# Performance work log

Hardware: AMD Instinct MI355X
Metric: run time of the kernel (lower is better)

Reference implementation:

```python
import jax, jax.numpy as jnp
import numpy as np

B = 524288   # particles
H = 128      # hidden_size
E = 64       # embed_dim
NT = 512     # num trajectories
IN = 16 + 9 + E  # fc1 input dim = 89
EPS = 1e-6


def setup_inputs() -> dict:
    key = jax.random.key(0)
    ks = jax.random.split(key, 12)
    w = lambda k, shp, fan_in: (jax.random.normal(k, shp, dtype=jnp.float32)
                                / np.sqrt(fan_in).astype(np.float32))
    return {
        "F": jax.random.normal(ks[0], (B, 3, 3), dtype=jnp.float32),
        "C": jax.random.normal(ks[1], (B, 3, 3), dtype=jnp.float32),
        "traj_id": 7,
        "latent": jax.random.normal(ks[2], (NT, E), dtype=jnp.float32),
        "W1": w(ks[3], (IN, H), IN), "b1": jnp.zeros((H,), jnp.float32),
        "W2": w(ks[4], (H, H), H),   "b2": jnp.zeros((H,), jnp.float32),
        "W3": w(ks[5], (H, H), H),   "b3": jnp.zeros((H,), jnp.float32),
        "W4": w(ks[6], (H, H), H),   "b4": jnp.zeros((H,), jnp.float32),
        "W5": w(ks[7], (H, H), H),   "b5": jnp.zeros((H,), jnp.float32),
        "W6": w(ks[8], (H, H), H),   "b6": jnp.zeros((H,), jnp.float32),
        "W7": w(ks[9], (H, 9), H),   "b7": jnp.zeros((9,), jnp.float32),
    }


def _strain_features(F):
    # FFt: [B,3,3]; J = clamp(det F); J1 = clamp(F00); sigma: 3 singular values
    FFt = jnp.einsum('bij,bkj->bik', F, F)
    J = jnp.maximum(jnp.linalg.det(F), EPS)
    J1 = jnp.maximum(F[:, 0, 0], EPS)
    sigma = jnp.linalg.svd(F, compute_uv=False)  # descending, like torch.svd
    return jnp.concatenate([
        FFt.reshape(-1, 9),
        jnp.log(J)[:, None], sigma, J[:, None],
        jnp.log(J1)[:, None], J1[:, None],
    ], axis=-1)  # [B,16]


def reference(F, C, traj_id, latent,
              W1, b1, W2, b2, W3, b3, W4, b4, W5, b5, W6, b6, W7, b7):
    strain = _strain_features(F)                                   # [B,16]
    lat = jnp.broadcast_to(latent[traj_id], (F.shape[0], latent.shape[1]))
    x = jnp.concatenate([strain, C.reshape(-1, 9), lat], axis=-1)  # [B,89]
    g = lambda z: jax.nn.gelu(z, approximate=False)  # exact, matches torch GELU
    x = g(x @ W1 + b1)
    x = g(x @ W2 + b2)
    x = g(x @ W3 + b3)
    x = g(x @ W4 + b4)
    x = g(x @ W5 + b5)
    x = g(x @ W6 + b6)
    out = (x @ W7 + b7).reshape(-1, 3, 3)
    return 0.5 * (out + jnp.swapaxes(out, 1, 2))  # symmetric stress [B,3,3]
```

## Files before the change

### kernel.cpp

```cpp
#include <hip/hip_runtime.h>
#include <hip/hip_bf16.h>
#include <math.h>

#define BPART   524288
#define NBLK    (BPART / 128)
#define W7_OFF  98304
#define WB_N    102400
#define BIAS_N  800
#define PREP_N  (WB_N + BIAS_N)

typedef __bf16 bf16x8 __attribute__((ext_vector_type(8)));
typedef float  f32x16 __attribute__((ext_vector_type(16)));
typedef float  f32x4  __attribute__((ext_vector_type(4)));
typedef float  f32x2  __attribute__((ext_vector_type(2)));

#define MFMA __builtin_amdgcn_mfma_f32_32x32x16_bf16
#define UNROLL _Pragma("unroll")

union XU { unsigned u[4]; bf16x8 v; };

__device__ __forceinline__ unsigned short f2bf(float f) {
  union { float f; unsigned u; } v; v.f = f;
  unsigned r = v.u + 0x7fffu + ((v.u >> 16) & 1u);
  return (unsigned short)(r >> 16);
}
__device__ __forceinline__ unsigned pack_bf16(float a, float b) {
  unsigned ua = __builtin_bit_cast(unsigned, a) + 0x8000u;
  unsigned ub = __builtin_bit_cast(unsigned, b) + 0x8000u;
  return __builtin_amdgcn_perm(ub, ua, 0x07060302u);
}

__device__ __forceinline__ int sigma(int n) {
  int c = ((n >> 5) << 2) | ((n >> 3) & 3);
  return ((c >> 1) << 4) | (((n >> 2) & 1) << 3) | ((c & 1) << 2) | (n & 3);
}

__device__ __forceinline__ f32x2 pk_mul(f32x2 a, f32x2 b) {
  f32x2 d; asm("v_pk_mul_f32 %0, %1, %2" : "=v"(d) : "v"(a), "v"(b)); return d;
}
__device__ __forceinline__ f32x2 pk_fma(f32x2 a, f32x2 b, f32x2 c) {
  f32x2 d; asm("v_pk_fma_f32 %0, %1, %2, %3" : "=v"(d) : "v"(a), "v"(b), "v"(c)); return d;
}
__device__ __forceinline__ f32x2 gelu2(f32x2 z) {
  const f32x2 c1 = {0.1029432f, 0.1029432f};
  const f32x2 c0 = {2.30220818f, 2.30220818f};
  f32x2 z2 = pk_mul(z, z);
  f32x2 t  = pk_fma(z2, c1, c0);
  f32x2 yp = pk_mul(z, t);
  float e0 = __builtin_amdgcn_exp2f(-yp.x);
  float e1 = __builtin_amdgcn_exp2f(-yp.y);
  float r0 = __builtin_amdgcn_rcpf(e0 + 1.0f);
  float r1 = __builtin_amdgcn_rcpf(e1 + 1.0f);
  f32x2 g; g.x = z.x * r0; g.y = z.y * r1;
  return g;
}
__device__ __forceinline__ void cp16(const void* g, void* l) {
  __builtin_amdgcn_global_load_lds(
      (const __attribute__((address_space(1))) void*)g,
      (__attribute__((address_space(3))) void*)l, 16, 0, 0);
}

__global__ void prep_weights(
    const float* __restrict__ W1, const float* __restrict__ W2,
    const float* __restrict__ W3, const float* __restrict__ W4,
    const float* __restrict__ W5, const float* __restrict__ W6,
    const float* __restrict__ W7,
    const float* __restrict__ b1, const float* __restrict__ b2,
    const float* __restrict__ b3, const float* __restrict__ b4,
    const float* __restrict__ b5, const float* __restrict__ b6,
    const float* __restrict__ b7,
    unsigned short* __restrict__ wsb, float* __restrict__ wsf)
{
  int idx = blockIdx.x * 256 + threadIdx.x;
  if (idx < WB_N) {
    unsigned short v = 0;
    if (idx < W7_OFF) {
      int l = idx >> 14;
      int o = idx & 16383;
      int n = o >> 7, e = o & 127;
      int k = (((e >> 3) ^ (n & 7)) << 3) | (e & 7);
      int sn = sigma(n);
      const float* W = (l==0)?W1:(l==1)?W2:(l==2)?W3:(l==3)?W4:(l==4)?W5:W6;
      float x = (l == 0) ? ((k < 89) ? W[k*128 + sn] : 0.0f)
                         : W[k*128 + sn];
      v = f2bf(x);
    } else {
      int o = idx - W7_OFF;
      int n = o >> 7, e = o & 127;
      int k = (((e >> 3) ^ (n & 7)) << 3) | (e & 7);
      int sn = sigma(n);
      v = (sn < 9) ? f2bf(W7[k*9 + sn]) : (unsigned short)0;
    }
    wsb[idx] = v;
  } else if (idx < PREP_N) {
    int r = idx - WB_N;
    float x;
    if (r < 768) {
      int l = r >> 7, n = r & 127;
      const float* bb = (l==0)?b1:(l==1)?b2:(l==2)?b3:(l==3)?b4:(l==4)?b5:b6;
      x = bb[sigma(n)];
    } else {
      int n = r - 768;
      int sn = sigma(n);
      x = (sn < 9) ? b7[sn] : 0.0f;
    }
    wsf[r] = x;
  }
}

#define MFMA_LAYER(NKK)                                                       \
  {                                                                           \
    const float* bls_ = (const float*)((const char*)wt_s + 32768);            \
    UNROLL                                                                    \
    for (int kk = 0; kk < (NKK); ++kk) {                                      \
      XU x_;                                                                  \
      x_.u[0] = xw[4*kk+0]; x_.u[1] = xw[4*kk+1];                             \
      x_.u[2] = xw[4*kk+2]; x_.u[3] = xw[4*kk+3];                             \
      const int ch_ = ((2*kk + lk) ^ x7) << 3;                                \
      UNROLL                                                                  \
      for (int tn = 0; tn < 4; ++tn) {                                        \
        bf16x8 w_ = *(const bf16x8*)&wt_s[tn*4096 + rb0 + ch_];               \
        if (kk == 0) {                                                        \
          f32x16 cf_;                                                         \
          UNROLL                                                              \
          for (int qq = 0; qq < 4; ++qq) {                                    \
            f32x4 b4_ = *(const f32x4*)&bls_[tn*32 + qq*8 + lk*4];            \
            cf_[4*qq+0] = b4_[0]; cf_[4*qq+1] = b4_[1];                       \
            cf_[4*qq+2] = b4_[2]; cf_[4*qq+3] = b4_[3];                       \
          }                                                                   \
          acc[tn] = MFMA(w_, x_.v, cf_, 0, 0, 0);                             \
        } else {                                                              \
          acc[tn] = MFMA(w_, x_.v, acc[tn], 0, 0, 0);                         \
        }                                                                     \
      }                                                                       \
    }                                                                         \
  }

#define GELU_EPILOGUE                                                         \
  UNROLL                                                                      \
  for (int c = 0; c < 16; ++c) {                                              \
    const int tn_ = c >> 2, q_ = c & 3, t_ = c >> 1, h_ = c & 1;              \
    f32x2 za_, zb_;                                                           \
    za_.x = acc[tn_][4*q_+0]; za_.y = acc[tn_][4*q_+1];                       \
    zb_.x = acc[tn_][4*q_+2]; zb_.y = acc[tn_][4*q_+3];                       \
    f32x2 ga_ = gelu2(za_);                                                   \
    f32x2 gb_ = gelu2(zb_);                                                   \
    xw[4*t_ + 2*h_ + 0] = pack_bf16(ga_.x, ga_.y);                            \
    xw[4*t_ + 2*h_ + 1] = pack_bf16(gb_.x, gb_.y);                            \
  }

__global__ __launch_bounds__(256, 4) void stress_mlp(
    const float* __restrict__ F, const float* __restrict__ Cmat,
    const int* __restrict__ traj, const float* __restrict__ latent,
    const unsigned short* __restrict__ wst, const float* __restrict__ wsf,
    float* __restrict__ out)
{
  __shared__ __align__(16) unsigned short wt_s[128 * 128 + 256];

  const int tid  = threadIdx.x;
  const int lane = tid & 63;
  const int wid  = tid >> 6;
  const int lm   = lane & 31;
  const int lk   = lane >> 5;
  const int x7   = lm & 7;
  const int rb0  = lm << 7;
  const int pbase = (int)blockIdx.x << 7;
  const int p    = pbase + (wid << 5) + lm;

  {
    const char* src = (const char*)wst;
    char* dst = (char*)wt_s;
    UNROLL
    for (int i = 0; i < 8; ++i)
      cp16(src + i*4096 + tid*16, dst + i*4096 + tid*16);
    if (tid < 32) cp16((const char*)wsf + tid*16, dst + 32768 + tid*16);
  }

  unsigned xw[32];

  {
    const float* Fp = F + (size_t)p * 9;
    float f[9];
    UNROLL
    for (int i = 0; i < 9; ++i) f[i] = Fp[i];
    float fft[9];
    UNROLL
    for (int i = 0; i < 3; ++i)
      UNROLL
      for (int k = 0; k < 3; ++k)
        fft[i*3+k] = f[i*3]*f[k*3] + f[i*3+1]*f[k*3+1] + f[i*3+2]*f[k*3+2];
    const float* lat = latent + (size_t)traj[0] * 64;

    if (lk == 0) {
      xw[0] = pack_bf16(fft[0], fft[1]);
      xw[1] = pack_bf16(fft[2], fft[3]);
      xw[2] = pack_bf16(fft[4], fft[5]);
      xw[3] = pack_bf16(fft[6], fft[7]);
      const float* Cp = Cmat + (size_t)p * 9;
      UNROLL
      for (int i = 0; i < 4; ++i) xw[4+i] = pack_bf16(Cp[2*i], Cp[2*i+1]);
      UNROLL
      for (int t = 0; t < 4; ++t) {
        const float* lb = lat + 7 + 16*t;
        UNROLL
        for (int i = 0; i < 4; ++i) xw[8 + 4*t + i] = pack_bf16(lb[2*i], lb[2*i+1]);
      }
    } else {
      float det = f[0]*(f[4]*f[8]-f[5]*f[7]) - f[1]*(f[3]*f[8]-f[5]*f[6])
                + f[2]*(f[3]*f[7]-f[4]*f[6]);
      float J  = fmaxf(det, 1e-6f);
      float J1 = fmaxf(f[0], 1e-6f);
      float a00=fft[0], a01=fft[1], a02=fft[2], a11=fft[4], a12=fft[5], a22=fft[8];
      float q  = (a00+a11+a22) * (1.0f/3.0f);
      float d0 = a00-q, d1 = a11-q, d2 = a22-q;
      float p2 = d0*d0 + d1*d1 + d2*d2 + 2.0f*(a01*a01 + a02*a02 + a12*a12);
      float e0, e1, e2;
      if (p2 < 1e-14f) { e0 = e1 = e2 = q; }
      else {
        float pp  = sqrtf(p2 * (1.0f/6.0f));
        float inv = 1.0f / pp;
        float b00=d0*inv, b11=d1*inv, b22=d2*inv, b01=a01*inv, b02=a02*inv, b12=a12*inv;
        float detb = b00*(b11*b22-b12*b12) - b01*(b01*b22-b12*b02) + b02*(b01*b12-b11*b02);
        float rr = 0.5f * detb;
        rr = fminf(fmaxf(rr, -1.0f), 1.0f);
        float pr = acosf(rr) * (1.0f / (3.0f * 6.2831853071795864f));
        e0 = q + 2.0f*pp*__builtin_amdgcn_cosf(pr);
        e2 = q + 2.0f*pp*__builtin_amdgcn_cosf(pr + (1.0f/3.0f));
        e1 = 3.0f*q - e0 - e2;
      }
      float s0 = sqrtf(fmaxf(e0, 0.f));
      float s1 = sqrtf(fmaxf(e1, 0.f));
      float s2 = sqrtf(fmaxf(e2, 0.f));
      xw[0] = pack_bf16(fft[8], logf(J));
      xw[1] = pack_bf16(s0, s1);
      xw[2] = pack_bf16(s2, J);
      xw[3] = pack_bf16(logf(J1), J1);
      float c8 = Cmat[(size_t)p*9 + 8];
      xw[4] = pack_bf16(c8, lat[0]);
      xw[5] = pack_bf16(lat[1], lat[2]);
      xw[6] = pack_bf16(lat[3], lat[4]);
      xw[7] = pack_bf16(lat[5], lat[6]);
      UNROLL
      for (int t = 0; t < 3; ++t) {
        const float* lb = lat + 15 + 16*t;
        UNROLL
        for (int i = 0; i < 4; ++i) xw[8 + 4*t + i] = pack_bf16(lb[2*i], lb[2*i+1]);
      }
      xw[20] = pack_bf16(lat[63], 0.0f);
      xw[21] = 0u; xw[22] = 0u; xw[23] = 0u;
    }
  }

  f32x16 acc[4];

  __syncthreads();
  MFMA_LAYER(6)
  __syncthreads();
  {
    const char* src = (const char*)(wst + (1 << 14));
    UNROLL
    for (int i = 0; i < 8; ++i)
      cp16(src + i*4096 + tid*16, (char*)wt_s + i*4096 + tid*16);
    if (tid < 32) cp16((const char*)(wsf + 128) + tid*16, (char*)wt_s + 32768 + tid*16);
  }
  GELU_EPILOGUE

  for (int l = 1; l < 6; ++l) {
    __syncthreads();
    MFMA_LAYER(8)
    __syncthreads();
    if (l < 5) {
      const char* src = (const char*)(wst + ((l + 1) << 14));
      UNROLL
      for (int i = 0; i < 8; ++i)
        cp16(src + i*4096 + tid*16, (char*)wt_s + i*4096 + tid*16);
      if (tid < 32)
        cp16((const char*)(wsf + ((l + 1) << 7)) + tid*16, (char*)wt_s + 32768 + tid*16);
    } else {
      const char* src = (const char*)(wst + W7_OFF);
      UNROLL
      for (int i = 0; i < 2; ++i)
        cp16(src + i*4096 + tid*16, (char*)wt_s + i*4096 + tid*16);
      if (tid < 8)
        cp16((const char*)(wsf + 768) + tid*16, (char*)wt_s + 32768 + tid*16);
    }
    GELU_EPILOGUE
  }

  __syncthreads();
  f32x16 a7;
  {
    const float* bls = (const float*)((const char*)wt_s + 32768);
    UNROLL
    for (int kk = 0; kk < 8; ++kk) {
      XU x;
      x.u[0] = xw[4*kk+0]; x.u[1] = xw[4*kk+1];
      x.u[2] = xw[4*kk+2]; x.u[3] = xw[4*kk+3];
      const int ch = ((2*kk + lk) ^ x7) << 3;
      bf16x8 w = *(const bf16x8*)&wt_s[rb0 + ch];
      if (kk == 0) {
        f32x16 cf;
        UNROLL
        for (int qq = 0; qq < 4; ++qq) {
          f32x4 b4 = *(const f32x4*)&bls[qq*8 + lk*4];
          cf[4*qq+0] = b4[0]; cf[4*qq+1] = b4[1];
          cf[4*qq+2] = b4[2]; cf[4*qq+3] = b4[3];
        }
        a7 = MFMA(w, x.v, cf, 0, 0, 0);
      } else {
        a7 = MFMA(w, x.v, a7, 0, 0, 0);
      }
    }
  }
  __syncthreads();

  float o8 = __shfl_xor(a7[0], 32);
  float* ots = (float*)wt_s;
  if (lk == 0) {
    const int row = (wid << 5) + lm;
    float z[9];
    UNROLL
    for (int i = 0; i < 8; ++i) z[i] = a7[i];
    z[8] = o8;
    UNROLL
    for (int rr = 0; rr < 3; ++rr)
      UNROLL
      for (int cc = 0; cc < 3; ++cc)
        ots[row*9 + rr*3 + cc] = 0.5f * (z[rr*3+cc] + z[cc*3+rr]);
  }
  __syncthreads();

  float4* dst = (float4*)(out + (size_t)pbase * 9);
  const float4* srcv = (const float4*)ots;
  for (int s = tid; s < 288; s += 256) dst[s] = srcv[s];
}

extern "C" void kernel_launch(void* const* d_in, const int* in_sizes, int n_in,
                              void* d_out, int out_size, void* d_ws, size_t ws_size,
                              hipStream_t stream) {
  const float* F   = (const float*)d_in[0];
  const float* C   = (const float*)d_in[1];
  const int*   trj = (const int*)d_in[2];
  const float* lat = (const float*)d_in[3];
  const float* W1  = (const float*)d_in[4];
  const float* b1  = (const float*)d_in[5];
  const float* W2  = (const float*)d_in[6];
  const float* b2  = (const float*)d_in[7];
  const float* W3  = (const float*)d_in[8];
  const float* b3  = (const float*)d_in[9];
  const float* W4  = (const float*)d_in[10];
  const float* b4  = (const float*)d_in[11];
  const float* W5  = (const float*)d_in[12];
  const float* b5  = (const float*)d_in[13];
  const float* W6  = (const float*)d_in[14];
  const float* b6  = (const float*)d_in[15];
  const float* W7  = (const float*)d_in[16];
  const float* b7  = (const float*)d_in[17];

  unsigned short* wsb = (unsigned short*)d_ws;
  float* wsf = (float*)((char*)d_ws + WB_N * 2);

  prep_weights<<<dim3((PREP_N + 255) / 256), dim3(256), 0, stream>>>(
      W1, W2, W3, W4, W5, W6, W7, b1, b2, b3, b4, b5, b6, b7, wsb, wsf);
  stress_mlp<<<dim3(NBLK), dim3(256), 0, stream>>>(
      F, C, trj, lat, wsb, wsf, (float*)d_out);
}
```

Baseline: 269.4 us.

## Double-buffer layer weights in LDS and double block size to 512 threads

Weight staging now uses two LDS buffers, so the next layer's weights and biases are copied into one buffer while MFMAs read the other. This removes one barrier per layer and hides global-to-LDS load latency behind compute. Blocks grow to 512 threads (256 particles), which halves the number of blocks and spreads each weight load over more particles. LDS use doubles to about 66 KB per block, and launch_bounds(512,4) may put pressure on occupancy and registers.

```diff
diff --git a/kernel.cpp b/kernel.cpp
--- a/kernel.cpp
+++ b/kernel.cpp
@@ -3,7 +3,7 @@
 #include <math.h>
 
 #define BPART   524288
-#define NBLK    (BPART / 128)
+#define NBLK    (BPART / 256)
 #define W7_OFF  98304
 #define WB_N    102400
 #define BIAS_N  800
@@ -13,11 +13,10 @@
 typedef float  f32x16 __attribute__((ext_vector_type(16)));
 typedef float  f32x4  __attribute__((ext_vector_type(4)));
 typedef float  f32x2  __attribute__((ext_vector_type(2)));
+typedef unsigned u32x4 __attribute__((ext_vector_type(4)));
 
 #define MFMA __builtin_amdgcn_mfma_f32_32x32x16_bf16
 #define UNROLL _Pragma("unroll")
-
-union XU { unsigned u[4]; bf16x8 v; };
 
 __device__ __forceinline__ unsigned short f2bf(float f) {
   union { float f; unsigned u; } v; v.f = f;
@@ -108,32 +107,36 @@
   }
 }
 
-#define MFMA_LAYER(NKK)                                                       \
-  {                                                                           \
-    const float* bls_ = (const float*)((const char*)wt_s + 32768);            \
+#define MFMA_PAIR(WPTR, BLS, T0, NKK)                                         \
+  UNROLL                                                                      \
+  for (int kk = 0; kk < (NKK); ++kk) {                                        \
+    bf16x8 x_ = __builtin_bit_cast(bf16x8, xw[kk]);                           \
+    const int ch_ = ((2*kk + lk) ^ x7) << 3;                                  \
     UNROLL                                                                    \
-    for (int kk = 0; kk < (NKK); ++kk) {                                      \
-      XU x_;                                                                  \
-      x_.u[0] = xw[4*kk+0]; x_.u[1] = xw[4*kk+1];                             \
-      x_.u[2] = xw[4*kk+2]; x_.u[3] = xw[4*kk+3];                             \
-      const int ch_ = ((2*kk + lk) ^ x7) << 3;                                \
-      UNROLL                                                                  \
-      for (int tn = 0; tn < 4; ++tn) {                                        \
-        bf16x8 w_ = *(const bf16x8*)&wt_s[tn*4096 + rb0 + ch_];               \
-        if (kk == 0) {                                                        \
-          f32x16 cf_;                                                         \
-          UNROLL                                                              \
-          for (int qq = 0; qq < 4; ++qq) {                                    \
-            f32x4 b4_ = *(const f32x4*)&bls_[tn*32 + qq*8 + lk*4];            \
-            cf_[4*qq+0] = b4_[0]; cf_[4*qq+1] = b4_[1];                       \
-            cf_[4*qq+2] = b4_[2]; cf_[4*qq+3] = b4_[3];                       \
-          }                                                                   \
-          acc[tn] = MFMA(w_, x_.v, cf_, 0, 0, 0);                             \
-        } else {                                                              \
-          acc[tn] = MFMA(w_, x_.v, acc[tn], 0, 0, 0);                         \
+    for (int t_ = 0; t_ < 2; ++t_) {                                          \
+      const int tn_ = (T0) + t_;                                              \
+      bf16x8 w_ = *(const bf16x8*)&(WPTR)[tn_*4096 + rb0 + ch_];              \
+      if (kk == 0) {                                                          \
+        f32x16 cf_;                                                           \
+        UNROLL                                                                \
+        for (int qq = 0; qq < 4; ++qq) {                                      \
+          f32x4 b4_ = *(const f32x4*)&(BLS)[tn_*32 + qq*8 + lk*4];            \
+          cf_[4*qq+0] = b4_[0]; cf_[4*qq+1] = b4_[1];                         \
+          cf_[4*qq+2] = b4_[2]; cf_[4*qq+3] = b4_[3];                         \
         }                                                                     \
+        acc[tn_] = MFMA(w_, x_, cf_, 0, 0, 0);                                \
+      } else {                                                                \
+        acc[tn_] = MFMA(w_, x_, acc[tn_], 0, 0, 0);                           \
       }                                                                       \
     }                                                                         \
+  }
+
+#define MFMA_LAYER(WPTR, NKK)                                                 \
+  {                                                                           \
+    const unsigned short* wp_ = (WPTR);                                       \
+    const float* bls_ = (const float*)((const char*)wp_ + 32768);             \
+    MFMA_PAIR(wp_, bls_, 0, NKK)                                              \
+    MFMA_PAIR(wp_, bls_, 2, NKK)                                              \
   }
 
 #define GELU_EPILOGUE                                                         \
@@ -145,17 +148,30 @@
     zb_.x = acc[tn_][4*q_+2]; zb_.y = acc[tn_][4*q_+3];                       \
     f32x2 ga_ = gelu2(za_);                                                   \
     f32x2 gb_ = gelu2(zb_);                                                   \
-    xw[4*t_ + 2*h_ + 0] = pack_bf16(ga_.x, ga_.y);                            \
-    xw[4*t_ + 2*h_ + 1] = pack_bf16(gb_.x, gb_.y);                            \
-  }
-
-__global__ __launch_bounds__(256, 4) void stress_mlp(
+    xw[t_][2*h_ + 0] = pack_bf16(ga_.x, ga_.y);                               \
+    xw[t_][2*h_ + 1] = pack_bf16(gb_.x, gb_.y);                               \
+  }
+
+#define STAGE_W(LOFF, BUFIDX)                                                 \
+  {                                                                           \
+    const char* s_ = (const char*)(wst + (LOFF));                             \
+    char* d_ = (char*)wbuf[BUFIDX];                                           \
+    UNROLL                                                                    \
+    for (int i_ = 0; i_ < 4; ++i_)                                            \
+      cp16(s_ + i_*8192 + tid*16, d_ + i_*8192 + tid*16);                     \
+  }
+#define STAGE_B(BOFF, BUFIDX, NT)                                             \
+  if (tid < (NT))                                                             \
+    cp16((const char*)(wsf + (BOFF)) + tid*16,                                \
+         (char*)wbuf[BUFIDX] + 32768 + tid*16);
+
+__global__ __launch_bounds__(512, 4) void stress_mlp(
     const float* __restrict__ F, const float* __restrict__ Cmat,
     const int* __restrict__ traj, const float* __restrict__ latent,
     const unsigned short* __restrict__ wst, const float* __restrict__ wsf,
     float* __restrict__ out)
 {
-  __shared__ __align__(16) unsigned short wt_s[128 * 128 + 256];
+  __shared__ __align__(16) unsigned short wbuf[2][16384 + 256];
 
   const int tid  = threadIdx.x;
   const int lane = tid & 63;
@@ -164,19 +180,13 @@
   const int lk   = lane >> 5;
   const int x7   = lm & 7;
   const int rb0  = lm << 7;
-  const int pbase = (int)blockIdx.x << 7;
+  const int pbase = (int)blockIdx.x << 8;
   const int p    = pbase + (wid << 5) + lm;
 
-  {
-    const char* src = (const char*)wst;
-    char* dst = (char*)wt_s;
-    UNROLL
-    for (int i = 0; i < 8; ++i)
-      cp16(src + i*4096 + tid*16, dst + i*4096 + tid*16);
-    if (tid < 32) cp16((const char*)wsf + tid*16, dst + 32768 + tid*16);
-  }
-
-  unsigned xw[32];
+  STAGE_W(0, 0)
+  STAGE_B(0, 0, 32)
+
+  u32x4 xw[8];
 
   {
     const float* Fp = F + (size_t)p * 9;
@@ -192,18 +202,18 @@
     const float* lat = latent + (size_t)traj[0] * 64;
 
     if (lk == 0) {
-      xw[0] = pack_bf16(fft[0], fft[1]);
-      xw[1] = pack_bf16(fft[2], fft[3]);
-      xw[2] = pack_bf16(fft[4], fft[5]);
-      xw[3] = pack_bf16(fft[6], fft[7]);
+      xw[0][0] = pack_bf16(fft[0], fft[1]);
+      xw[0][1] = pack_bf16(fft[2], fft[3]);
+      xw[0][2] = pack_bf16(fft[4], fft[5]);
+      xw[0][3] = pack_bf16(fft[6], fft[7]);
       const float* Cp = Cmat + (size_t)p * 9;
       UNROLL
-      for (int i = 0; i < 4; ++i) xw[4+i] = pack_bf16(Cp[2*i], Cp[2*i+1]);
+      for (int i = 0; i < 4; ++i) xw[1][i] = pack_bf16(Cp[2*i], Cp[2*i+1]);
       UNROLL
       for (int t = 0; t < 4; ++t) {
         const float* lb = lat + 7 + 16*t;
         UNROLL
-        for (int i = 0; i < 4; ++i) xw[8 + 4*t + i] = pack_bf16(lb[2*i], lb[2*i+1]);
+        for (int i = 0; i < 4; ++i) xw[2+t][i] = pack_bf16(lb[2*i], lb[2*i+1]);
       }
     } else {
       float det = f[0]*(f[4]*f[8]-f[5]*f[7]) - f[1]*(f[3]*f[8]-f[5]*f[6])
@@ -231,73 +241,72 @@
       float s0 = sqrtf(fmaxf(e0, 0.f));
       float s1 = sqrtf(fmaxf(e1, 0.f));
       float s2 = sqrtf(fmaxf(e2, 0.f));
-      xw[0] = pack_bf16(fft[8], logf(J));
-      xw[1] = pack_bf16(s0, s1);
-      xw[2] = pack_bf16(s2, J);
-      xw[3] = pack_bf16(logf(J1), J1);
+      xw[0][0] = pack_bf16(fft[8], logf(J));
+      xw[0][1] = pack_bf16(s0, s1);
+      xw[0][2] = pack_bf16(s2, J);
+      xw[0][3] = pack_bf16(logf(J1), J1);
       float c8 = Cmat[(size_t)p*9 + 8];
-      xw[4] = pack_bf16(c8, lat[0]);
-      xw[5] = pack_bf16(lat[1], lat[2]);
-      xw[6] = pack_bf16(lat[3], lat[4]);
-      xw[7] = pack_bf16(lat[5], lat[6]);
+      xw[1][0] = pack_bf16(c8, lat[0]);
+      xw[1][1] = pack_bf16(lat[1], lat[2]);
+      xw[1][2] = pack_bf16(lat[3], lat[4]);
+      xw[1][3] = pack_bf16(lat[5], lat[6]);
       UNROLL
       for (int t = 0; t < 3; ++t) {
         const float* lb = lat + 15 + 16*t;
         UNROLL
-        for (int i = 0; i < 4; ++i) xw[8 + 4*t + i] = pack_bf16(lb[2*i], lb[2*i+1]);
+        for (int i = 0; i < 4; ++i) xw[2+t][i] = pack_bf16(lb[2*i], lb[2*i+1]);
       }
-      xw[20] = pack_bf16(lat[63], 0.0f);
-      xw[21] = 0u; xw[22] = 0u; xw[23] = 0u;
+      xw[5][0] = pack_bf16(lat[63], 0.0f);
+      xw[5][1] = 0u; xw[5][2] = 0u; xw[5][3] = 0u;
     }
   }
 
   f32x16 acc[4];
 
   __syncthreads();
-  MFMA_LAYER(6)
-  __syncthreads();
+  STAGE_W(1 << 14, 1) STAGE_B(128, 1, 32)
+  MFMA_LAYER(wbuf[0], 6)
+  GELU_EPILOGUE
+  __syncthreads();
+
+  STAGE_W(2 << 14, 0) STAGE_B(256, 0, 32)
+  MFMA_LAYER(wbuf[1], 8)
+  GELU_EPILOGUE
+  __syncthreads();
+
+  STAGE_W(3 << 14, 1) STAGE_B(384, 1, 32)
+  MFMA_LAYER(wbuf[0], 8)
+  GELU_EPILOGUE
+  __syncthreads();
+
+  STAGE_W(4 << 14, 0) STAGE_B(512, 0, 32)
+  MFMA_LAYER(wbuf[1], 8)
+  GELU_EPILOGUE
+  __syncthreads();
+
+  STAGE_W(5 << 14, 1) STAGE_B(640, 1, 32)
+  MFMA_LAYER(wbuf[0], 8)
+  GELU_EPILOGUE
+  __syncthreads();
+
   {
-    const char* src = (const char*)(wst + (1 << 14));
-    UNROLL
-    for (int i = 0; i < 8; ++i)
-      cp16(src + i*4096 + tid*16, (char*)wt_s + i*4096 + tid*16);
-    if (tid < 32) cp16((const char*)(wsf + 128) + tid*16, (char*)wt_s + 32768 + tid*16);
-  }
-  GELU_EPILOGUE
-
-  for (int l = 1; l < 6; ++l) {
-    __syncthreads();
-    MFMA_LAYER(8)
-    __syncthreads();
-    if (l < 5) {
-      const char* src = (const char*)(wst + ((l + 1) << 14));
-      UNROLL
-      for (int i = 0; i < 8; ++i)
-        cp16(src + i*4096 + tid*16, (char*)wt_s + i*4096 + tid*16);
-      if (tid < 32)
-        cp16((const char*)(wsf + ((l + 1) << 7)) + tid*16, (char*)wt_s + 32768 + tid*16);
-    } else {
-      const char* src = (const char*)(wst + W7_OFF);
-      UNROLL
-      for (int i = 0; i < 2; ++i)
-        cp16(src + i*4096 + tid*16, (char*)wt_s + i*4096 + tid*16);
-      if (tid < 8)
-        cp16((const char*)(wsf + 768) + tid*16, (char*)wt_s + 32768 + tid*16);
-    }
-    GELU_EPILOGUE
-  }
-
-  __syncthreads();
+    const char* s_ = (const char*)(wst + W7_OFF);
+    cp16(s_ + tid*16, (char*)wbuf[0] + tid*16);
+    STAGE_B(768, 0, 8)
+  }
+  MFMA_LAYER(wbuf[1], 8)
+  GELU_EPILOGUE
+  __syncthreads();
+
   f32x16 a7;
   {
-    const float* bls = (const float*)((const char*)wt_s + 32768);
+    const unsigned short* wp = wbuf[0];
+    const float* bls = (const float*)((const char*)wp + 32768);
     UNROLL
     for (int kk = 0; kk < 8; ++kk) {
-      XU x;
-      x.u[0] = xw[4*kk+0]; x.u[1] = xw[4*kk+1];
-      x.u[2] = xw[4*kk+2]; x.u[3] = xw[4*kk+3];
+      bf16x8 x = __builtin_bit_cast(bf16x8, xw[kk]);
       const int ch = ((2*kk + lk) ^ x7) << 3;
-      bf16x8 w = *(const bf16x8*)&wt_s[rb0 + ch];
+      bf16x8 w = *(const bf16x8*)&wp[rb0 + ch];
       if (kk == 0) {
         f32x16 cf;
         UNROLL
@@ -306,16 +315,15 @@
           cf[4*qq+0] = b4[0]; cf[4*qq+1] = b4[1];
           cf[4*qq+2] = b4[2]; cf[4*qq+3] = b4[3];
         }
-        a7 = MFMA(w, x.v, cf, 0, 0, 0);
+        a7 = MFMA(w, x, cf, 0, 0, 0);
       } else {
-        a7 = MFMA(w, x.v, a7, 0, 0, 0);
+        a7 = MFMA(w, x, a7, 0, 0, 0);
       }
     }
   }
-  __syncthreads();
 
   float o8 = __shfl_xor(a7[0], 32);
-  float* ots = (float*)wt_s;
+  float* ots = (float*)wbuf[1];
   if (lk == 0) {
     const int row = (wid << 5) + lm;
     float z[9];
@@ -332,7 +340,8 @@
 
   float4* dst = (float4*)(out + (size_t)pbase * 9);
   const float4* srcv = (const float4*)ots;
-  for (int s = tid; s < 288; s += 256) dst[s] = srcv[s];
+  UNROLL
+  for (int s = tid; s < 576; s += 512) dst[s] = srcv[s];
 }
 
 extern "C" void kernel_launch(void* const* d_in, const int* in_sizes, int n_in,
@@ -362,6 +371,6 @@
 
   prep_weights<<<dim3((PREP_N + 255) / 256), dim3(256), 0, stream>>>(
       W1, W2, W3, W4, W5, W6, W7, b1, b2, b3, b4, b5, b6, b7, wsb, wsf);
-  stress_mlp<<<dim3(NBLK), dim3(256), 0, stream>>>(
+  stress_mlp<<<dim3(NBLK), dim3(512), 0, stream>>>(
       F, C, trj, lat, wsb, wsf, (float*)d_out);
 }
```

After: 283.5 us. 5.2% more time.
